# Performance work log

Measured on AMD Instinct MI355X. Metric: run time of the kernel, lower is better.

The kernel has to match this reference:

```python
import jax, jax.numpy as jnp
import numpy as np
from jax import lax

B_SZ, D_SPEC, P, NC, MLP_D = 4096, 30, 9, 64, 64
L = P * P + 1  # 82 tokens (81 spiral + cls)


def _spiral_idx(patch=P):
    # Replicates Scan.forward's hardcoded assignments_map: center pixel, then
    # concentric rings (top row, right col, bottom row, left col), each of length 2r.
    cen = patch // 2
    rows, cols = [cen], [cen]
    for r in range(1, cen + 1):
        rows += [cen - r] * (2 * r); cols += list(range(cen - r + 1, cen + r + 1))
        rows += list(range(cen - r + 1, cen + r + 1)); cols += [cen + r] * (2 * r)
        rows += [cen + r] * (2 * r); cols += list(range(cen - r, cen + r))
        rows += list(range(cen - r, cen + r)); cols += [cen - r] * (2 * r)
    return np.asarray(rows), np.asarray(cols)

_ROWS, _COLS = _spiral_idx()


def _ln(x, g, b, eps=1e-5):
    m = x.mean(-1, keepdims=True)
    v = ((x - m) ** 2).mean(-1, keepdims=True)
    return (x - m) * lax.rsqrt(v + eps) * g + b


def _bn(x, g, b, m, v, nspatial, eps=1e-5):
    sh = (1, -1) + (1,) * nspatial
    return (x - m.reshape(sh)) * lax.rsqrt(v.reshape(sh) + eps) * g.reshape(sh) + b.reshape(sh)


def setup_inputs():
    key = jax.random.key(0)
    ks = iter(jax.random.split(key, 40))
    def rn(shape, s=0.1):
        return s * jax.random.normal(next(ks), shape, jnp.float32)
    return {
        "input_data": jax.random.normal(next(ks), (B_SZ, 1, D_SPEC, P, P), jnp.float32),
        "w3": rn((8, 1, 3, 3, 3)), "b3": rn((8,)),
        "g3": 1.0 + rn((8,)), "be3": rn((8,)), "m3": jnp.zeros((8,)), "v3": jnp.ones((8,)),
        "w2c": rn((NC, 8 * D_SPEC, 3, 3)), "b2c": rn((NC,)),
        "g2": 1.0 + rn((NC,)), "be2": rn((NC,)), "m2": jnp.zeros((NC,)), "v2": jnp.ones((NC,)),
        "pos_emb": rn((1, L, NC)), "cls_tok": rn((1, 1, NC)),
        "ln1_g": jnp.ones((NC,)), "ln1_b": jnp.zeros((NC,)),
        "Wb": rn((NC, NC)), "bb": rn((NC,)),
        "Wc": rn((NC, NC)), "bc": rn((NC,)),
        "Wd": rn((NC, NC)), "bd": rn((NC,)),
        "delta_p": rn((1, L, NC)), "A_p": rn((L, NC)),
        "Wst": rn((NC, NC)), "bst": rn((NC,)), "bias_st": rn((1, 1, NC)),
        "ln2_g": jnp.ones((NC,)), "ln2_b": jnp.zeros((NC,)),
        "Wm1": rn((NC, MLP_D)), "bm1": rn((MLP_D,)),
        "Wm2": rn((MLP_D, NC)), "bm2": rn((NC,)),
    }


def _forward(input_data, w3, b3, g3, be3, m3, v3, w2c, b2c, g2, be2, m2, v2,
             pos_emb, cls_tok, ln1_g, ln1_b, Wb, bb, Wc, bc, Wd, bd,
             delta_p, A_p, Wst, bst, bias_st, ln2_g, ln2_b, Wm1, bm1, Wm2, bm2):
    b = input_data.shape[0]
    # conv3d (SAME, k=3) + BN(eval) + ReLU
    h = lax.conv_general_dilated(input_data, w3, (1, 1, 1), [(1, 1)] * 3,
                                 dimension_numbers=("NCDHW", "OIDHW", "NCDHW"))
    h = jax.nn.relu(_bn(h + b3[None, :, None, None, None], g3, be3, m3, v3, 3))
    h = h.reshape(b, 8 * D_SPEC, P, P)  # 'b c h w y -> b (c h) w y'
    # conv2d (SAME, k=3) + BN(eval) + ReLU
    h = lax.conv_general_dilated(h, w2c, (1, 1), [(1, 1)] * 2,
                                 dimension_numbers=("NCHW", "OIHW", "NCHW"))
    h = jax.nn.relu(_bn(h + b2c[None, :, None, None], g2, be2, m2, v2, 2))
    # spiral scan gather: [B,C,H,W] -> [B,81,C]
    seq = jnp.transpose(h, (0, 2, 3, 1))[:, _ROWS, _COLS, :]
    tok = jnp.concatenate([jnp.broadcast_to(cls_tok, (b, 1, NC)), seq], axis=1) + pos_emb
    # (emb dropout = identity in eval)
    # --- Residual(LayerNormalize(S6_noC)) ---
    xn = _ln(tok, ln1_g, ln1_b)
    z = jax.nn.sigmoid(xn)
    B0 = xn @ Wb + bb
    C_ = xn @ Wc + bc
    sq = jnp.mean(xn, axis=1, keepdims=True)              # SToken squeeze [B,1,D]
    sq = jax.nn.sigmoid(jax.nn.relu(sq @ Wst + bst))
    T_ = (sq + bias_st) * xn                              # [B,L,D]
    delta = jax.nn.sigmoid(xn @ Wd + bd + delta_p)
    A_ = delta * A_p[None]                                # [B,L,D]
    Bx = delta * B0 * xn                                  # B_ * x fused
    def step(s, inp):
        a, bx, c, t = inp
        s = a * s + bx
        return s, c * s + t
    ins = (jnp.moveaxis(A_, 1, 0), jnp.moveaxis(Bx, 1, 0),
           jnp.moveaxis(C_, 1, 0), jnp.moveaxis(T_, 1, 0))  # [L,B,D]
    _, out = lax.scan(step, jnp.zeros((b, NC), xn.dtype), ins)
    tok = tok + jnp.moveaxis(out, 0, 1) * z               # residual
    # AdaptiveAvgPool1d(1) over seq + squeeze -> [B, D]
    pooled = tok.mean(axis=1)
    # --- Residual(LayerNormalize(MLP_Block)) (dropout = identity) ---
    yn = _ln(pooled, ln2_g, ln2_b)
    mlp = jax.nn.gelu(yn @ Wm1 + bm1, approximate=False) @ Wm2 + bm2
    return pooled + mlp


def reference(input_data, w3, b3, g3, be3, m3, v3, w2c, b2c, g2, be2, m2, v2,
              pos_emb, cls_tok, ln1_g, ln1_b, Wb, bb, Wc, bc, Wd, bd,
              delta_p, A_p, Wst, bst, bias_st, ln2_g, ln2_b, Wm1, bm1, Wm2, bm2):
    return _forward(input_data, w3, b3, g3, be3, m3, v3, w2c, b2c, g2, be2, m2, v2,
                    pos_emb, cls_tok, ln1_g, ln1_b, Wb, bb, Wc, bc, Wd, bd,
                    delta_p, A_p, Wst, bst, bias_st, ln2_g, ln2_b, Wm1, bm1, Wm2, bm2)
```

## Files before the change

kernel.cpp:

```cpp
#include <hip/hip_runtime.h>

typedef unsigned short u16;
typedef unsigned int u32;
typedef __attribute__((ext_vector_type(8))) short bf16x8;
typedef __attribute__((ext_vector_type(4))) float f32x4;
typedef __attribute__((ext_vector_type(4))) int i32x4;

#define DEV __device__ __forceinline__

DEV u16 f2bf(float f){
  unsigned u = __float_as_uint(f);
  u += 0x7fffu + ((u >> 16) & 1u);
  return (u16)(u >> 16);
}
DEV float bf2f(u16 h){ return __uint_as_float(((unsigned)h) << 16); }

DEV int spiral_t(int pix){
  int px = pix / 9, py = pix % 9;
  int dr = px - 4, dc = py - 4;
  int ar = dr < 0 ? -dr : dr, ac = dc < 0 ? -dc : dc;
  int r = ar > ac ? ar : ac;
  if (r == 0) return 0;
  int start = 1 + 4*r*(r-1);
  if (dr == -r && dc >= -r+1) return start + dc + r - 1;
  if (dc == r)  return start + 2*r + dr + r - 1;
  if (dr == r)  return start + 4*r + dc + r;
  return start + 6*r + dr + r;
}

__global__ __launch_bounds__(256) void k_wt(const float* __restrict__ w2c,
                                            const float* __restrict__ g2,
                                            const float* __restrict__ v2,
                                            u16* __restrict__ Wt2){
  int idx = blockIdx.x*256 + threadIdx.x;
  if (idx >= 72*64*32) return;
  int kk = idx & 31;
  int o  = (idx >> 5) & 63;
  int tile = idx >> 11;
  int dxy = tile >> 3;
  int chunk = tile & 7;
  int ch = chunk*32 + kk;
  float v = 0.f;
  if (ch < 240){
    float s2 = g2[o] * rsqrtf(v2[o] + 1e-5f);
    v = w2c[(o*240 + ch)*9 + dxy] * s2;
  }
  Wt2[idx] = f2bf(v);
}

__global__ __launch_bounds__(256) void k_conv3d(const float* __restrict__ x,
    const float* __restrict__ w3, const float* __restrict__ b3,
    const float* __restrict__ g3, const float* __restrict__ be3,
    const float* __restrict__ m3, const float* __restrict__ v3,
    u16* __restrict__ h1){
  __shared__ float tile[3993];
  __shared__ float wle[216];
  __shared__ float sc[8], sh[8];
  int b = blockIdx.x, tid = threadIdx.x;
  for (int i = tid; i < 3993; i += 256) tile[i] = 0.f;
  if (tid < 216) wle[tid] = w3[tid];
  if (tid < 8){
    float s = g3[tid]*rsqrtf(v3[tid]+1e-5f);
    sc[tid] = s;
    sh[tid] = (b3[tid]-m3[tid])*s + be3[tid];
  }
  __syncthreads();
  const float* xin = x + b*2430;
  for (int i = tid; i < 2430; i += 256){
    int dd = i / 81, rem = i % 81;
    int px = rem / 9, py = rem % 9;
    tile[(dd+1)*121 + (px+1)*11 + (py+1)] = xin[i];
  }
  __syncthreads();
  u16* hb = h1 + (size_t)b*19440;

  for (int col = tid; col < 648; col += 256){
    int pix = col >> 3, co = col & 7;
    int px = pix / 9, py = pix % 9;
    const float* base = tile + px*11 + py;
    float wp[27];
    #pragma unroll
    for (int q=0;q<27;q++) wp[q] = wle[co*27+q];
    float scv = sc[co], shv = sh[co];

    float s0[9], s1[9], s2[9];
#define LSL(S, SL)                                                            \
    { const float* tp2 = base + (SL)*121;                                     \
      _Pragma("unroll")                                                       \
      for (int kx=0;kx<3;kx++)                                                \
        _Pragma("unroll")                                                     \
        for (int ky=0;ky<3;ky++) S[kx*3+ky] = tp2[kx*11+ky]; }
#define DOT3(A, SA, SB, SC)                                                   \
    { A = 0.f;                                                                \
      _Pragma("unroll")                                                       \
      for (int q=0;q<9;q++) A = fmaf(SA[q], wp[q], A);                        \
      _Pragma("unroll")                                                       \
      for (int q=0;q<9;q++) A = fmaf(SB[q], wp[9+q], A);                      \
      _Pragma("unroll")                                                       \
      for (int q=0;q<9;q++) A = fmaf(SC[q], wp[18+q], A); }

    LSL(s0, 0); LSL(s1, 1); LSL(s2, 2);
    u16 outv[30];
    #pragma unroll
    for (int d3 = 0; d3 < 30; d3 += 3){
      float a;
      DOT3(a, s0, s1, s2);
      outv[d3] = f2bf(fmaxf(fmaf(a, scv, shv), 0.f));
      LSL(s0, d3+3);
      DOT3(a, s1, s2, s0);
      outv[d3+1] = f2bf(fmaxf(fmaf(a, scv, shv), 0.f));
      LSL(s1, d3+4);
      DOT3(a, s2, s0, s1);
      outv[d3+2] = f2bf(fmaxf(fmaf(a, scv, shv), 0.f));
      LSL(s2, d3+5);
    }
#undef LSL
#undef DOT3
    u32* dst = (u32*)(hb + pix*240 + co*30);
    #pragma unroll
    for (int q=0;q<15;q++) dst[q] = ((u32)outv[2*q+1] << 16) | (u32)outv[2*q];
  }
}

__global__ __launch_bounds__(256, 2) void k_conv2d(const u16* __restrict__ h1,
    const u16* __restrict__ Wt2,
    const float* __restrict__ b2c, const float* __restrict__ g2,
    const float* __restrict__ be2, const float* __restrict__ m2,
    const float* __restrict__ v2,
    const float* __restrict__ pos_emb, const float* __restrict__ cls_tok,
    const float* __restrict__ ln1_g, const float* __restrict__ ln1_b,
    const float* __restrict__ Wst, const float* __restrict__ bst,
    const float* __restrict__ bias_st,
    u16* __restrict__ xn, float* __restrict__ tsum, float* __restrict__ sqs){
  __shared__ __align__(16) char smem[80848];
  const int ZROW = 80352;
  int tid = threadIdx.x;
  int wv = tid >> 6, ln = tid & 63;
  int lq = ln >> 4, lr = ln & 15;
  int img0 = blockIdx.x*2;
  size_t grow0 = (size_t)img0*81;

  int bln = lr*32 + lq*8;

#define LOADB(TAP, C, B)                                                        \
    { const u16* Bt_ = Wt2 + (TAP)*16384 + bln;                                 \
      _Pragma("unroll")                                                         \
      for (int kk=0;kk<2;kk++)                                                  \
        _Pragma("unroll")                                                       \
        for (int j=0;j<4;j++)                                                   \
          B[kk][j] = *(const bf16x8*)(Bt_ + ((C)*2+kk)*2048 + j*512); }

  bf16x8 bB0[2][4], bB1[2][4], bB2[2][4];
  LOADB(0, 0, bB0);
  LOADB(0, 1, bB1);
  LOADB(0, 2, bB2);

  for (int r = tid; r < 162; r += 256)
    *(i32x4*)(smem + r*496 + 480) = (i32x4){0,0,0,0};
  if (tid < 31) *(i32x4*)(smem + ZROW + tid*16) = (i32x4){0,0,0,0};
  {
    const u16* src = h1 + grow0*240;
    for (int idx = tid; idx < 162*30; idx += 256){
      int r = idx / 30, c = idx % 30;
      *(i32x4*)(smem + r*496 + c*16) = *(const i32x4*)(src + idx*8);
    }
  }
  __syncthreads();

  f32x4 acc[3][4];
  #pragma unroll
  for (int i=0;i<3;i++)
    #pragma unroll
    for (int j=0;j<4;j++) acc[i][j] = (f32x4){0.f,0.f,0.f,0.f};

#define CALCADDR(TAP, A0, A1, A13)                                              \
  { int dx = (TAP)/3 - 1, dy = (TAP)%3 - 1;                                     \
    _Pragma("unroll")                                                           \
    for (int rt=0;rt<3;rt++){                                                   \
      int row = (wv*3+rt)*16 + lr;                                              \
      int pix = row % 81;                                                       \
      int px = pix/9, py = pix%9;                                               \
      int px2 = px + dx, py2 = py + dy;                                         \
      bool valid = (row < 162) && ((unsigned)px2 < 9u) && ((unsigned)py2 < 9u); \
      int nrow = (row - pix) + px2*9 + py2;                                     \
      int base = valid ? nrow*496 : ZROW;                                       \
      A0[rt]  = base + lq*16;                                                   \
      A1[rt]  = base + 64 + lq*16;                                              \
      A13[rt] = (lq == 3) ? ZROW : (A1[rt] + 384);                              \
    } }

#define LOADA(C, SA0, SA1, SA13, A0, A1)                                        \
    { _Pragma("unroll")                                                         \
      for (int rt=0;rt<3;rt++){                                                 \
        A0[rt] = *(const bf16x8*)(smem + SA0[rt] + (C)*128);                    \
        A1[rt] = *(const bf16x8*)(smem + ((C)==3 ? SA13[rt]                     \
                                                 : SA1[rt] + (C)*128)); } }

#define DOMFMA(B, A0, A1)                                                       \
    { __builtin_amdgcn_s_setprio(1);                                            \
      _Pragma("unroll")                                                         \
      for (int rt=0;rt<3;rt++)                                                  \
        _Pragma("unroll")                                                       \
        for (int j=0;j<4;j++)                                                   \
          acc[rt][j] = __builtin_amdgcn_mfma_f32_16x16x32_bf16(A0[rt], B[0][j], acc[rt][j], 0, 0, 0); \
      _Pragma("unroll")                                                         \
      for (int rt=0;rt<3;rt++)                                                  \
        _Pragma("unroll")                                                       \
        for (int j=0;j<4;j++)                                                   \
          acc[rt][j] = __builtin_amdgcn_mfma_f32_16x16x32_bf16(A1[rt], B[1][j], acc[rt][j], 0, 0, 0); \
      __builtin_amdgcn_s_setprio(0); }

#define TAPBODY(TAPV, BA, BB, BC)                                               \
  { int ntap_ = (TAPV) < 8 ? (TAPV)+1 : 8;                                      \
    DOMFMA(BA, aAX0, aAX1);                                                     \
    LOADB((TAPV), 3, BA); LOADA(2, aC0, aC1, aC13, aAX0, aAX1);                 \
    DOMFMA(BB, aAY0, aAY1);                                                     \
    LOADB(ntap_, 0, BB); CALCADDR(ntap_, aN0, aN1, aN13);                       \
    LOADA(3, aC0, aC1, aC13, aAY0, aAY1);                                       \
    DOMFMA(BC, aAX0, aAX1);                                                     \
    LOADB(ntap_, 1, BC); LOADA(0, aN0, aN1, aN13, aAX0, aAX1);                  \
    DOMFMA(BA, aAY0, aAY1);                                                     \
    LOADB(ntap_, 2, BA); LOADA(1, aN0, aN1, aN13, aAY0, aAY1);                  \
    _Pragma("unroll")                                                           \
    for (int rt=0;rt<3;rt++){ aC0[rt]=aN0[rt]; aC1[rt]=aN1[rt]; aC13[rt]=aN13[rt]; } }

  int aC0[3], aC1[3], aC13[3];
  int aN0[3], aN1[3], aN13[3];
  bf16x8 aAX0[3], aAX1[3], aAY0[3], aAY1[3];

  CALCADDR(0, aC0, aC1, aC13);
  LOADA(0, aC0, aC1, aC13, aAX0, aAX1);
  LOADA(1, aC0, aC1, aC13, aAY0, aAY1);

  for (int t3 = 0; t3 < 9; t3 += 3){
    TAPBODY(t3+0, bB0, bB1, bB2);
    TAPBODY(t3+1, bB1, bB2, bB0);
    TAPBODY(t3+2, bB2, bB0, bB1);
  }
#undef CALCADDR
#undef LOADB
#undef LOADA
#undef DOMFMA
#undef TAPBODY

  __syncthreads();

  float t2c[4], lg[4], lb[4];
  #pragma unroll
  for (int j=0;j<4;j++){
    int col = j*16 + lr;
    float s2 = g2[col]*rsqrtf(v2[col]+1e-5f);
    t2c[j] = (b2c[col]-m2[col])*s2 + be2[col];
    lg[j] = ln1_g[col]; lb[j] = ln1_b[col];
  }

  float st0[4]={0,0,0,0}, st1[4]={0,0,0,0};
  float sx0[4]={0,0,0,0}, sx1[4]={0,0,0,0};

  #pragma unroll
  for (int rt=0;rt<3;rt++){
    #pragma unroll
    for (int e=0;e<4;e++){
      int row = (wv*3+rt)*16 + lq*4 + e;
      if (row < 162){
        int im = (row >= 81);
        int pix = row - im*81;
        int tsp = spiral_t(pix);
        const float* pe = pos_emb + (1+tsp)*64;
        float y[4], m1 = 0.f, m2v = 0.f;
        #pragma unroll
        for (int j=0;j<4;j++){
          y[j] = fmaxf(acc[rt][j][e] + t2c[j], 0.f) + pe[j*16+lr];
          m1 += y[j]; m2v = fmaf(y[j], y[j], m2v);
        }
        #pragma unroll
        for (int off=1; off<16; off<<=1){
          m1  += __shfl_xor(m1,  off, 64);
          m2v += __shfl_xor(m2v, off, 64);
        }
        float mean = m1*(1.f/64.f);
        float var  = m2v*(1.f/64.f) - mean*mean;
        float rs = rsqrtf(var + 1e-5f);
        u16* dst = xn + ((size_t)(img0+im)*82 + 1 + tsp)*64;
        #pragma unroll
        for (int j=0;j<4;j++){
          float xnv = (y[j]-mean)*rs*lg[j] + lb[j];
          dst[j*16+lr] = f2bf(xnv);
          if (im == 0){ st0[j] += y[j]; sx0[j] += xnv; }
          else        { st1[j] += y[j]; sx1[j] += xnv; }
        }
      }
    }
  }

  #pragma unroll
  for (int j=0;j<4;j++){
    st0[j] += __shfl_xor(st0[j],16,64); st0[j] += __shfl_xor(st0[j],32,64);
    st1[j] += __shfl_xor(st1[j],16,64); st1[j] += __shfl_xor(st1[j],32,64);
    sx0[j] += __shfl_xor(sx0[j],16,64); sx0[j] += __shfl_xor(sx0[j],32,64);
    sx1[j] += __shfl_xor(sx1[j],16,64); sx1[j] += __shfl_xor(sx1[j],32,64);
  }
  float* partT = (float*)smem;
  float* partX = (float*)(smem + 2048);
  float* xsumL = (float*)(smem + 4096);
  if (lq == 0){
    #pragma unroll
    for (int j=0;j<4;j++){
      partT[wv*128 +       j*16+lr] = st0[j];
      partT[wv*128 + 64  + j*16+lr] = st1[j];
      partX[wv*128 +       j*16+lr] = sx0[j];
      partX[wv*128 + 64  + j*16+lr] = sx1[j];
    }
  }
  __syncthreads();
  if (tid < 128){
    int im = tid >> 6, d = tid & 63;
    float tt = partT[im*64+d] + partT[128+im*64+d] + partT[256+im*64+d] + partT[384+im*64+d];
    float xx = partX[im*64+d] + partX[128+im*64+d] + partX[256+im*64+d] + partX[384+im*64+d];
    float clsv = cls_tok[d] + pos_emb[d];
    float c1v = clsv, c2v = clsv*clsv;
    #pragma unroll
    for (int off=1; off<64; off<<=1){ c1v += __shfl_xor(c1v, off, 64); c2v += __shfl_xor(c2v, off, 64); }
    float cm = c1v*(1.f/64.f), cv = c2v*(1.f/64.f) - cm*cm;
    float cxn = (clsv - cm)*rsqrtf(cv + 1e-5f)*ln1_g[d] + ln1_b[d];
    xn[((size_t)(img0+im)*82)*64 + d] = f2bf(cxn);
    tsum[(size_t)(img0+im)*64 + d] = tt + clsv;
    xsumL[im*64 + d] = (xx + cxn) * (1.f/82.f);
  }
  __syncthreads();
  {
    int im = tid >> 7, d2 = tid & 127;
    int d = d2 >> 1, half = d2 & 1;
    float a = 0.f;
    int k0 = half*32;
    #pragma unroll
    for (int k=0;k<32;k++) a = fmaf(xsumL[im*64 + k0+k], Wst[(k0+k)*64+d], a);
    a += __shfl_xor(a, 1, 64);
    if (half == 0){
      a += bst[d];
      a = fmaxf(a, 0.f);
      a = 1.f/(1.f + __expf(-a));
      sqs[(size_t)(img0+im)*64 + d] = a + bias_st[d];
    }
  }
}

__global__ __launch_bounds__(256, 2) void k_fuse(const u16* __restrict__ xn,
    const float* __restrict__ tsum, const float* __restrict__ sqs,
    const float* __restrict__ Wb, const float* __restrict__ Wc, const float* __restrict__ Wd,
    const float* __restrict__ bbv, const float* __restrict__ bcv, const float* __restrict__ bdv,
    const float* __restrict__ delta_p, const float* __restrict__ A_p,
    const float* __restrict__ ln2_g, const float* __restrict__ ln2_b,
    const float* __restrict__ Wm1, const float* __restrict__ bm1,
    const float* __restrict__ Wm2, const float* __restrict__ bm2,
    float* __restrict__ out){
  __shared__ __align__(16) char xnL[96*128];
  __shared__ u16 AxL[96][66], BxL[96][66], CxL[96][66];
  int tid = threadIdx.x;
  int wv = tid >> 6, ln = tid & 63;
  int lq = ln >> 4, lr = ln & 15;
  int b = blockIdx.x;

  bf16x8 bfr[3][2];
  {
    int cc = wv*16 + lr;
    const float* Ws[3] = {Wb, Wc, Wd};
    #pragma unroll
    for (int w=0;w<3;w++)
      #pragma unroll
      for (int kk=0;kk<2;kk++){
        int k0 = kk*32 + lq*8;
        bf16x8 f;
        #pragma unroll
        for (int e=0;e<8;e++) f[e] = (short)f2bf(Ws[w][(k0+e)*64 + cc]);
        bfr[w][kk] = f;
      }
  }

  {
    const u16* src = xn + (size_t)b*82*64;
    for (int idx = tid; idx < 656; idx += 256){
      int r = idx >> 3, c = idx & 7;
      *(i32x4*)(xnL + r*128 + ((c*16) ^ ((r&7)<<4))) = *(const i32x4*)(src + idx*8);
    }
    for (int idx = tid; idx < 112; idx += 256){
      int r = 82 + (idx >> 3), c = idx & 7;
      *(i32x4*)(xnL + r*128 + ((c*16) ^ ((r&7)<<4))) = (i32x4){0,0,0,0};
    }
  }
  __syncthreads();

  f32x4 acc[6][3];
  #pragma unroll
  for (int i=0;i<6;i++)
    #pragma unroll
    for (int w=0;w<3;w++) acc[i][w] = (f32x4){0.f,0.f,0.f,0.f};

  #pragma unroll
  for (int rt=0;rt<6;rt++){
    int row = rt*16 + lr;
    bf16x8 afr[2];
    #pragma unroll
    for (int kk=0;kk<2;kk++)
      afr[kk] = *(const bf16x8*)(xnL + row*128 + ((kk*64 + lq*16) ^ ((row&7)<<4)));
    #pragma unroll
    for (int kk=0;kk<2;kk++)
      #pragma unroll
      for (int w=0;w<3;w++)
        acc[rt][w] = __builtin_amdgcn_mfma_f32_16x16x32_bf16(afr[kk], bfr[w][kk], acc[rt][w], 0, 0, 0);
  }

  {
    int d = wv*16 + lr;
    float bB = bbv[d], bC = bcv[d], bD = bdv[d];
    #pragma unroll
    for (int rt=0;rt<6;rt++){
      #pragma unroll
      for (int e=0;e<4;e++){
        int t = rt*16 + lq*4 + e;
        if (t < 82){
          float B0 = acc[rt][0][e] + bB;
          float Cv = acc[rt][1][e] + bC;
          float Dr = acc[rt][2][e] + bD + delta_p[t*64+d];
          float D  = 1.f/(1.f + __expf(-Dr));
          float xv = bf2f(*(const u16*)(xnL + t*128 + ((d*2) ^ ((t&7)<<4))));
          AxL[t][d] = f2bf(D * A_p[t*64+d]);
          BxL[t][d] = f2bf(D * B0 * xv);
          CxL[t][d] = f2bf(Cv);
        }
      }
    }
  }
  __syncthreads();

  if (wv == 0){
    int d = ln;
    float sq = sqs[(size_t)b*64 + d];
    float s = 0.f, racc = 0.f;
    for (int t = 0; t < 82; t++){
      float a  = bf2f(AxL[t][d]);
      float bx = bf2f(BxL[t][d]);
      float c  = bf2f(CxL[t][d]);
      float xv = bf2f(*(const u16*)(xnL + t*128 + ((d*2) ^ ((t&7)<<4))));
      s = fmaf(a, s, bx);
      float o = fmaf(c, s, sq*xv);
      float z = 1.f/(1.f + __expf(-xv));
      racc = fmaf(o, z, racc);
    }
    float pooled = (tsum[(size_t)b*64 + d] + racc) * (1.f/82.f);
    float s1 = pooled, s2v = pooled*pooled;
    #pragma unroll
    for (int off=32; off>0; off>>=1){ s1 += __shfl_xor(s1, off, 64); s2v += __shfl_xor(s2v, off, 64); }
    float mean = s1*(1.f/64.f), var = s2v*(1.f/64.f) - mean*mean;
    float yn = (pooled - mean)*rsqrtf(var + 1e-5f)*ln2_g[d] + ln2_b[d];
    float a1 = bm1[d];
    for (int k=0;k<64;k++) a1 = fmaf(__shfl(yn, k, 64), Wm1[k*64+d], a1);
    float hg = 0.5f*a1*(1.f + erff(a1*0.70710678118654752f));
    float a2 = bm2[d];
    for (int k=0;k<64;k++) a2 = fmaf(__shfl(hg, k, 64), Wm2[k*64+d], a2);
    out[(size_t)b*64 + d] = pooled + a2;
  }
}

extern "C" void kernel_launch(void* const* d_in, const int* in_sizes, int n_in,
                              void* d_out, int out_size, void* d_ws, size_t ws_size,
                              hipStream_t stream){
  const float* x       = (const float*)d_in[0];
  const float* w3      = (const float*)d_in[1];
  const float* b3      = (const float*)d_in[2];
  const float* g3      = (const float*)d_in[3];
  const float* be3     = (const float*)d_in[4];
  const float* m3      = (const float*)d_in[5];
  const float* v3      = (const float*)d_in[6];
  const float* w2c     = (const float*)d_in[7];
  const float* b2c     = (const float*)d_in[8];
  const float* g2      = (const float*)d_in[9];
  const float* be2     = (const float*)d_in[10];
  const float* m2      = (const float*)d_in[11];
  const float* v2      = (const float*)d_in[12];
  const float* pos_emb = (const float*)d_in[13];
  const float* cls_tok = (const float*)d_in[14];
  const float* ln1_g   = (const float*)d_in[15];
  const float* ln1_b   = (const float*)d_in[16];
  const float* Wb      = (const float*)d_in[17];
  const float* bbv     = (const float*)d_in[18];
  const float* Wc      = (const float*)d_in[19];
  const float* bc      = (const float*)d_in[20];
  const float* Wd      = (const float*)d_in[21];
  const float* bd      = (const float*)d_in[22];
  const float* delta_p = (const float*)d_in[23];
  const float* A_p     = (const float*)d_in[24];
  const float* Wst     = (const float*)d_in[25];
  const float* bst     = (const float*)d_in[26];
  const float* bias_st = (const float*)d_in[27];
  const float* ln2_g   = (const float*)d_in[28];
  const float* ln2_b   = (const float*)d_in[29];
  const float* Wm1     = (const float*)d_in[30];
  const float* bm1     = (const float*)d_in[31];
  const float* Wm2     = (const float*)d_in[32];
  const float* bm2     = (const float*)d_in[33];

  char* ws = (char*)d_ws;
  u16*   h1   = (u16*)ws;
  u16*   Wt2  = (u16*)(ws + 159252480);
  u16*   xnb  = (u16*)(ws + 159571968);
  float* tsum = (float*)(ws + 202563584);
  float* sqs  = (float*)(ws + 203612160);

  k_wt    <<<576,  256, 0, stream>>>(w2c, g2, v2, Wt2);
  k_conv3d<<<4096, 256, 0, stream>>>(x, w3, b3, g3, be3, m3, v3, h1);
  k_conv2d<<<2048, 256, 0, stream>>>(h1, Wt2, b2c, g2, be2, m2, v2,
                                     pos_emb, cls_tok, ln1_g, ln1_b,
                                     Wst, bst, bias_st, xnb, tsum, sqs);
  k_fuse  <<<4096, 256, 0, stream>>>(xnb, tsum, sqs, Wb, Wc, Wd, bbv, bc, bd,
                                     delta_p, A_p, ln2_g, ln2_b,
                                     Wm1, bm1, Wm2, bm2, (float*)d_out);
}
```

Baseline: 364.6 us.

## Fuse conv3d into conv2d kernel, computing h1 directly into shared memory

Measured after the change: 733.7 us. 101% more time.

```diff
diff --git a/kernel.cpp b/kernel.cpp
--- a/kernel.cpp
+++ b/kernel.cpp
@@ -48,81 +48,10 @@
   Wt2[idx] = f2bf(v);
 }
 
-__global__ __launch_bounds__(256) void k_conv3d(const float* __restrict__ x,
+__global__ __launch_bounds__(256, 2) void k_cv23(const float* __restrict__ x,
     const float* __restrict__ w3, const float* __restrict__ b3,
     const float* __restrict__ g3, const float* __restrict__ be3,
     const float* __restrict__ m3, const float* __restrict__ v3,
-    u16* __restrict__ h1){
-  __shared__ float tile[3993];
-  __shared__ float wle[216];
-  __shared__ float sc[8], sh[8];
-  int b = blockIdx.x, tid = threadIdx.x;
-  for (int i = tid; i < 3993; i += 256) tile[i] = 0.f;
-  if (tid < 216) wle[tid] = w3[tid];
-  if (tid < 8){
-    float s = g3[tid]*rsqrtf(v3[tid]+1e-5f);
-    sc[tid] = s;
-    sh[tid] = (b3[tid]-m3[tid])*s + be3[tid];
-  }
-  __syncthreads();
-  const float* xin = x + b*2430;
-  for (int i = tid; i < 2430; i += 256){
-    int dd = i / 81, rem = i % 81;
-    int px = rem / 9, py = rem % 9;
-    tile[(dd+1)*121 + (px+1)*11 + (py+1)] = xin[i];
-  }
-  __syncthreads();
-  u16* hb = h1 + (size_t)b*19440;
-
-  for (int col = tid; col < 648; col += 256){
-    int pix = col >> 3, co = col & 7;
-    int px = pix / 9, py = pix % 9;
-    const float* base = tile + px*11 + py;
-    float wp[27];
-    #pragma unroll
-    for (int q=0;q<27;q++) wp[q] = wle[co*27+q];
-    float scv = sc[co], shv = sh[co];
-
-    float s0[9], s1[9], s2[9];
-#define LSL(S, SL)                                                            \
-    { const float* tp2 = base + (SL)*121;                                     \
-      _Pragma("unroll")                                                       \
-      for (int kx=0;kx<3;kx++)                                                \
-        _Pragma("unroll")                                                     \
-        for (int ky=0;ky<3;ky++) S[kx*3+ky] = tp2[kx*11+ky]; }
-#define DOT3(A, SA, SB, SC)                                                   \
-    { A = 0.f;                                                                \
-      _Pragma("unroll")                                                       \
-      for (int q=0;q<9;q++) A = fmaf(SA[q], wp[q], A);                        \
-      _Pragma("unroll")                                                       \
-      for (int q=0;q<9;q++) A = fmaf(SB[q], wp[9+q], A);                      \
-      _Pragma("unroll")                                                       \
-      for (int q=0;q<9;q++) A = fmaf(SC[q], wp[18+q], A); }
-
-    LSL(s0, 0); LSL(s1, 1); LSL(s2, 2);
-    u16 outv[30];
-    #pragma unroll
-    for (int d3 = 0; d3 < 30; d3 += 3){
-      float a;
-      DOT3(a, s0, s1, s2);
-      outv[d3] = f2bf(fmaxf(fmaf(a, scv, shv), 0.f));
-      LSL(s0, d3+3);
-      DOT3(a, s1, s2, s0);
-      outv[d3+1] = f2bf(fmaxf(fmaf(a, scv, shv), 0.f));
-      LSL(s1, d3+4);
-      DOT3(a, s2, s0, s1);
-      outv[d3+2] = f2bf(fmaxf(fmaf(a, scv, shv), 0.f));
-      LSL(s2, d3+5);
-    }
-#undef LSL
-#undef DOT3
-    u32* dst = (u32*)(hb + pix*240 + co*30);
-    #pragma unroll
-    for (int q=0;q<15;q++) dst[q] = ((u32)outv[2*q+1] << 16) | (u32)outv[2*q];
-  }
-}
-
-__global__ __launch_bounds__(256, 2) void k_conv2d(const u16* __restrict__ h1,
     const u16* __restrict__ Wt2,
     const float* __restrict__ b2c, const float* __restrict__ g2,
     const float* __restrict__ be2, const float* __restrict__ m2,
@@ -138,7 +67,6 @@
   int wv = tid >> 6, ln = tid & 63;
   int lq = ln >> 4, lr = ln & 15;
   int img0 = blockIdx.x*2;
-  size_t grow0 = (size_t)img0*81;
 
   int bln = lr*32 + lq*8;
 
@@ -158,12 +86,67 @@
   for (int r = tid; r < 162; r += 256)
     *(i32x4*)(smem + r*496 + 480) = (i32x4){0,0,0,0};
   if (tid < 31) *(i32x4*)(smem + ZROW + tid*16) = (i32x4){0,0,0,0};
-  {
-    const u16* src = h1 + grow0*240;
-    for (int idx = tid; idx < 162*30; idx += 256){
-      int r = idx / 30, c = idx % 30;
-      *(i32x4*)(smem + r*496 + c*16) = *(const i32x4*)(src + idx*8);
-    }
+
+  for (int c = tid; c < 1296; c += 256){
+    int img = c / 648, rem = c % 648;
+    int pix = rem >> 3, co = rem & 7;
+    int px = pix / 9, py = pix % 9;
+    const float* xin = x + (size_t)(img0+img)*2430 + px*9 + py;
+    int offs[9]; bool okf[9];
+    #pragma unroll
+    for (int kx=0;kx<3;kx++)
+      #pragma unroll
+      for (int ky=0;ky<3;ky++){
+        int q = kx*3+ky;
+        okf[q]  = ((unsigned)(px+kx-1) < 9u) && ((unsigned)(py+ky-1) < 9u);
+        offs[q] = (kx-1)*9 + (ky-1);
+      }
+    float wp[27];
+    #pragma unroll
+    for (int q=0;q<27;q++) wp[q] = w3[co*27+q];
+    float scv = g3[co]*rsqrtf(v3[co]+1e-5f);
+    float shv = (b3[co]-m3[co])*scv + be3[co];
+
+    float s0[9], s1[9], s2[9];
+#define LSLG(S, DD2)                                                          \
+    { int dd2_ = (DD2);                                                       \
+      if ((unsigned)dd2_ < 30u){                                              \
+        const float* xr_ = xin + dd2_*81;                                     \
+        _Pragma("unroll")                                                     \
+        for (int q=0;q<9;q++) S[q] = okf[q] ? xr_[offs[q]] : 0.f;             \
+      } else {                                                                \
+        _Pragma("unroll")                                                     \
+        for (int q=0;q<9;q++) S[q] = 0.f;                                     \
+      } }
+#define DOT3(A, SA, SB, SC)                                                   \
+    { A = 0.f;                                                                \
+      _Pragma("unroll")                                                       \
+      for (int q=0;q<9;q++) A = fmaf(SA[q], wp[q], A);                        \
+      _Pragma("unroll")                                                       \
+      for (int q=0;q<9;q++) A = fmaf(SB[q], wp[9+q], A);                      \
+      _Pragma("unroll")                                                       \
+      for (int q=0;q<9;q++) A = fmaf(SC[q], wp[18+q], A); }
+
+    LSLG(s0, -1); LSLG(s1, 0); LSLG(s2, 1);
+    u16 outv[30];
+    #pragma unroll
+    for (int d3 = 0; d3 < 30; d3 += 3){
+      float a;
+      DOT3(a, s0, s1, s2);
+      outv[d3] = f2bf(fmaxf(fmaf(a, scv, shv), 0.f));
+      LSLG(s0, d3+2);
+      DOT3(a, s1, s2, s0);
+      outv[d3+1] = f2bf(fmaxf(fmaf(a, scv, shv), 0.f));
+      LSLG(s1, d3+3);
+      DOT3(a, s2, s0, s1);
+      outv[d3+2] = f2bf(fmaxf(fmaf(a, scv, shv), 0.f));
+      LSLG(s2, d3+4);
+    }
+#undef LSLG
+#undef DOT3
+    u32* orow = (u32*)(smem + (img*81+pix)*496 + co*60);
+    #pragma unroll
+    for (int q=0;q<15;q++) orow[q] = ((u32)outv[2*q+1] << 16) | (u32)outv[2*q];
   }
   __syncthreads();
 
@@ -501,18 +484,17 @@
   const float* bm2     = (const float*)d_in[33];
 
   char* ws = (char*)d_ws;
-  u16*   h1   = (u16*)ws;
   u16*   Wt2  = (u16*)(ws + 159252480);
   u16*   xnb  = (u16*)(ws + 159571968);
   float* tsum = (float*)(ws + 202563584);
   float* sqs  = (float*)(ws + 203612160);
 
-  k_wt    <<<576,  256, 0, stream>>>(w2c, g2, v2, Wt2);
-  k_conv3d<<<4096, 256, 0, stream>>>(x, w3, b3, g3, be3, m3, v3, h1);
-  k_conv2d<<<2048, 256, 0, stream>>>(h1, Wt2, b2c, g2, be2, m2, v2,
-                                     pos_emb, cls_tok, ln1_g, ln1_b,
-                                     Wst, bst, bias_st, xnb, tsum, sqs);
-  k_fuse  <<<4096, 256, 0, stream>>>(xnb, tsum, sqs, Wb, Wc, Wd, bbv, bc, bd,
-                                     delta_p, A_p, ln2_g, ln2_b,
-                                     Wm1, bm1, Wm2, bm2, (float*)d_out);
+  k_wt   <<<576,  256, 0, stream>>>(w2c, g2, v2, Wt2);
+  k_cv23 <<<2048, 256, 0, stream>>>(x, w3, b3, g3, be3, m3, v3, Wt2,
+                                    b2c, g2, be2, m2, v2,
+                                    pos_emb, cls_tok, ln1_g, ln1_b,
+                                    Wst, bst, bias_st, xnb, tsum, sqs);
+  k_fuse <<<4096, 256, 0, stream>>>(xnb, tsum, sqs, Wb, Wc, Wd, bbv, bc, bd,
+                                    delta_p, A_p, ln2_g, ln2_b,
+                                    Wm1, bm1, Wm2, bm2, (float*)d_out);
 }
```
